# Kernel optimization log

Measured on AMD Instinct MI355X. Metric: run time of the kernel, lower is better.

Reference implementation:

```python
import jax, jax.numpy as jnp
import numpy as np
from jax import lax

KS, STRIDE, DIL, PAD = 3, 1, 1, 1
B, C_IN, C_OUT, D = 1, 16, 16, 64
K = KS ** 3


def setup_inputs():
    key = jax.random.key(0)
    k1, k2, k3 = jax.random.split(key, 3)
    x = jax.random.normal(k1, (B, C_IN, D, D, D), jnp.float32)
    std = 1.0 / float(np.sqrt(C_IN * K))
    kernel = jax.random.uniform(k2, (K, C_IN, C_OUT), jnp.float32, -std, std)
    # module zero-inits pkernel; use small random values so interp path is exercised
    pkernel = jax.random.normal(k3, (K, C_IN, 3 * K), jnp.float32) * 0.01
    return {"x": x, "kernel": kernel, "pkernel": pkernel}


def _deform_conv3d(x, kernel, pkernel):
    Bn, C, Dd, H, W = x.shape
    Kt = kernel.shape[0]
    # offset-predicting conv: pkernel [K, C_in, 3K] -> conv weight [3K, C_in, kd, kh, kw]
    w_off = jnp.transpose(pkernel.reshape(KS, KS, KS, C, 3 * Kt), (4, 3, 0, 1, 2))
    off = lax.conv_general_dilated(
        x, w_off, (STRIDE,) * 3, [(PAD, PAD)] * 3,
        rhs_dilation=(DIL,) * 3,
        dimension_numbers=("NCDHW", "OIDHW", "NCDHW"))
    Do, Ho, Wo = off.shape[2], off.shape[3], off.shape[4]
    off = off.reshape(Bn, Kt, 3, Do, Ho, Wo)  # 3 offset coords per kernel tap

    # base sampling grid: out_pos*stride - pad + tap*dilation, then add predicted offset
    r = jnp.arange(KS)
    tap = jnp.stack(jnp.meshgrid(r, r, r, indexing="ij"), -1).reshape(Kt, 3) * DIL - PAD
    gz = (jnp.arange(Do) * STRIDE).astype(x.dtype)
    gy = (jnp.arange(Ho) * STRIDE).astype(x.dtype)
    gx = (jnp.arange(Wo) * STRIDE).astype(x.dtype)
    cz = gz[None, None, :, None, None] + tap[None, :, 0, None, None, None] + off[:, :, 0]
    cy = gy[None, None, None, :, None] + tap[None, :, 1, None, None, None] + off[:, :, 1]
    cx = gx[None, None, None, None, :] + tap[None, :, 2, None, None, None] + off[:, :, 2]

    x_flat = x.reshape(Bn, C, Dd * H * W)

    def gather(idx):  # idx [B,K,Do,Ho,Wo] int32 -> [B,C,K,Do,Ho,Wo]
        g = jax.vmap(lambda xf, ix: xf[:, ix.reshape(-1)])(x_flat, idx)
        return g.reshape(Bn, C, Kt, Do, Ho, Wo)

    z0f = jnp.floor(cz); y0f = jnp.floor(cy); x0f = jnp.floor(cx)
    fz, fy, fx = cz - z0f, cy - y0f, cx - x0f
    z0 = z0f.astype(jnp.int32); y0 = y0f.astype(jnp.int32); x0 = x0f.astype(jnp.int32)

    # trilinear interp: accumulate 8 corners (zero outside volume)
    acc = jnp.zeros((Bn, C, Kt, Do, Ho, Wo), x.dtype)
    for dz in (0, 1):
        for dy in (0, 1):
            for dx in (0, 1):
                zi, yi, xi = z0 + dz, y0 + dy, x0 + dx
                valid = ((zi >= 0) & (zi < Dd) & (yi >= 0) & (yi < H)
                         & (xi >= 0) & (xi < W)).astype(x.dtype)
                w = ((fz if dz else 1.0 - fz) * (fy if dy else 1.0 - fy)
                     * (fx if dx else 1.0 - fx)) * valid
                idx = (jnp.clip(zi, 0, Dd - 1) * (H * W)
                       + jnp.clip(yi, 0, H - 1) * W + jnp.clip(xi, 0, W - 1))
                acc = acc + gather(idx) * w[:, None]

    # weighted sum over taps: kernel [K, C_in, C_out]
    return jnp.einsum("bckdhw,kco->bodhw", acc, kernel)


def reference(x, kernel, pkernel):
    return _deform_conv3d(x, kernel, pkernel)
```

## Files before the change

### kernel.cpp

```cpp
#include <hip/hip_runtime.h>

#define D 64
#define DD 4096
#define DDD 262144
#define K 27

typedef _Float16 half8  __attribute__((ext_vector_type(8)));
typedef _Float16 half2v __attribute__((ext_vector_type(2)));
typedef float    f32x4  __attribute__((ext_vector_type(4)));
typedef float    f32x2  __attribute__((ext_vector_type(2)));
typedef float    f32x16 __attribute__((ext_vector_type(16)));

#define HX 12
#define HY 8
#define HZ 6
#define HROW 12
#define HPLN 96
#define HSP  576
#define CPAD 24

#define WSW_CH (14*6*64)
#define KSW_CH (27*64)
#define KSW_OFF 88064

__device__ inline half2v h2of(half8 v, int d) {
    half2v r; r.x = v[2*d]; r.y = v[2*d+1]; return r;
}

__global__ __launch_bounds__(256) void prep_weights(const float* __restrict__ pk,
                                                    const float* __restrict__ kern,
                                                    _Float16* __restrict__ Wsw,
                                                    _Float16* __restrict__ Ksw) {
    int t = blockIdx.x * 256 + threadIdx.x;
    if (t < WSW_CH) {
        int lane = t & 63;
        int sm = t >> 6;
        int s = sm / 6, mt = sm - 6 * s;
        int m = mt * 16 + (lane & 15);
        int q = lane >> 4;
        half8 w;
#pragma unroll
        for (int j = 0; j < 8; ++j) {
            int k = 32 * s + 8 * q + j;
            int kt = k >> 4, c = k & 15;
            float wv = (kt < K && m < 81) ? pk[kt * 1296 + c * 81 + m] : 0.0f;
            w[j] = (_Float16)wv;
        }
        *(half8*)(Wsw + t * 8) = w;
    } else if (t < WSW_CH + KSW_CH) {
        int u = t - WSW_CH;
        int kt = u >> 6, lane = u & 63;
        int m = lane & 31, kh = lane >> 5;
        half8 w;
#pragma unroll
        for (int j = 0; j < 8; ++j) {
            int c = kh * 8 + j;
            float wv = (m < 16) ? kern[kt * 256 + c * 16 + m] : 0.0f;
            w[j] = (_Float16)wv;
        }
        *(half8*)(Ksw + u * 8) = w;
    }
}

__global__ __launch_bounds__(256, 4) void deform_main(
    const float* __restrict__ x,
    const _Float16* __restrict__ Wsw,
    const _Float16* __restrict__ Ksw,
    float* __restrict__ out)
{
    __shared__ _Float16 s_h[HSP * CPAD];
    __shared__ _Float16 s_off[81 * 64];

    const int tid  = threadIdx.x;
    const int lane = tid & 63;
    const int wave = __builtin_amdgcn_readfirstlane(tid >> 6);

    const int bx0 = blockIdx.x * 8;
    const int by0 = blockIdx.y * 4;
    const int bz0 = blockIdx.z * 2;

    for (int i = tid; i < HSP; i += 256) {
        int z = i / HPLN;
        int r = i - z * HPLN;
        int y = r / HROW;
        int xx = r - y * HROW;
        int gz = bz0 - 2 + z, gy = by0 - 2 + y, gx = bx0 - 2 + xx;
        bool in = (unsigned)gz < D && (unsigned)gy < D && (unsigned)gx < D;
        half8 a = {}, b = {};
        if (in) {
            const float* p = x + (gz * DD + gy * D + gx);
#pragma unroll
            for (int c = 0; c < 8; ++c) a[c] = (_Float16)p[c * DDD];
#pragma unroll
            for (int c = 0; c < 8; ++c) b[c] = (_Float16)p[(c + 8) * DDD];
        }
        *(half8*)(s_h + i * CPAD)     = a;
        *(half8*)(s_h + i * CPAD + 8) = b;
    }
    __syncthreads();

    {
        const int n = lane & 15, q = lane >> 4;
        const int vtz = wave >> 1;
        const int vty = 2 * (wave & 1) + (n >> 3);
        const int vtx = n & 7;
        f32x4 acc[6] = {};
        for (int s = 0; s < 14; ++s) {
            int kt = 2 * s + (q >> 1);
            int ktc = (kt < K) ? kt : 0;
            int kd = ktc / 9, kh = (ktc / 3) % 3, kw = ktc % 3;
            int idx = (vtz + kd + 1) * HPLN + (vty + kh + 1) * HROW + (vtx + kw + 1);
            half8 bfrag = *(const half8*)(s_h + idx * CPAD + (q & 1) * 8);
#pragma unroll
            for (int mt = 0; mt < 6; ++mt) {
                half8 afrag = *(const half8*)(Wsw + ((s * 6 + mt) * 64 + lane) * 8);
                acc[mt] = __builtin_amdgcn_mfma_f32_16x16x32_f16(afrag, bfrag, acc[mt], 0, 0, 0);
            }
        }
        const int v = wave * 16 + n;
#pragma unroll
        for (int mt = 0; mt < 6; ++mt)
#pragma unroll
            for (int r = 0; r < 4; ++r) {
                int o = mt * 16 + q * 4 + r;
                if (o < 81) s_off[o * 64 + v] = (_Float16)acc[mt][r];
            }
    }
    __syncthreads();

    const int l31 = lane & 31, lh = lane >> 5;
    const int h = wave & 1;
    const int kpar = wave >> 1;
    const int v = h * 32 + l31;
    const int tx = v & 7, ty = (v >> 3) & 3, tz = h;
    const int gz = bz0 + tz, gy = by0 + ty, gx = bx0 + tx;

    f32x16 acc2 = {};

    for (int k2 = 0; k2 < 14; ++k2) {
        const int kt = 2 * k2 + kpar;
        if (kt >= K) break;
        const int kd = kt / 9, kh = (kt / 3) % 3, kw = kt % 3;
        float cz = (float)(gz + kd - 1) + (float)s_off[(3 * kt + 0) * 64 + v];
        float cy = (float)(gy + kh - 1) + (float)s_off[(3 * kt + 1) * 64 + v];
        float cx = (float)(gx + kw - 1) + (float)s_off[(3 * kt + 2) * 64 + v];
        float zf = floorf(cz), yf = floorf(cy), xf = floorf(cx);
        float fz = cz - zf, fy = cy - yf, fx = cx - xf;
        int z0 = (int)zf, y0 = (int)yf, x0 = (int)xf;
        int hz0 = z0 - bz0 + 2, hy0 = y0 - by0 + 2, hx0 = x0 - bx0 + 2;

        half2v val2[4] = {};
        if ((unsigned)hz0 < (unsigned)(HZ - 1) && (unsigned)hy0 < (unsigned)(HY - 1)
            && (unsigned)hx0 < (unsigned)(HX - 1)) {
#pragma unroll
            for (int dz = 0; dz < 2; ++dz) {
                float wz = dz ? fz : 1.0f - fz;
#pragma unroll
                for (int dy = 0; dy < 2; ++dy) {
                    float wzy = wz * (dy ? fy : 1.0f - fy);
#pragma unroll
                    for (int dx = 0; dx < 2; ++dx) {
                        float w = wzy * (dx ? fx : 1.0f - fx);
                        int idx = (hz0 + dz) * HPLN + (hy0 + dy) * HROW + (hx0 + dx);
                        half8 cc = *(const half8*)(s_h + idx * CPAD + lh * 8);
                        _Float16 wh = (_Float16)w;
                        half2v w2; w2.x = wh; w2.y = wh;
#pragma unroll
                        for (int d = 0; d < 4; ++d)
                            val2[d] += w2 * h2of(cc, d);
                    }
                }
            }
        } else {
            f32x2 valf[4] = {};
#pragma unroll
            for (int dz = 0; dz < 2; ++dz) {
                int zi = z0 + dz;
                float wz = dz ? fz : 1.0f - fz;
#pragma unroll
                for (int dy = 0; dy < 2; ++dy) {
                    int yi = y0 + dy;
                    float wzy = wz * (dy ? fy : 1.0f - fy);
#pragma unroll
                    for (int dx = 0; dx < 2; ++dx) {
                        int xi = x0 + dx;
                        if ((unsigned)zi < D && (unsigned)yi < D && (unsigned)xi < D) {
                            float w = wzy * (dx ? fx : 1.0f - fx);
                            int base = zi * DD + yi * D + xi;
#pragma unroll
                            for (int d = 0; d < 4; ++d) {
                                valf[d].x += w * x[(lh * 8 + 2 * d)     * DDD + base];
                                valf[d].y += w * x[(lh * 8 + 2 * d + 1) * DDD + base];
                            }
                        }
                    }
                }
            }
#pragma unroll
            for (int d = 0; d < 4; ++d) {
                val2[d].x = (_Float16)valf[d].x;
                val2[d].y = (_Float16)valf[d].y;
            }
        }

        half8 bf;
#pragma unroll
        for (int d = 0; d < 4; ++d) { bf[2*d] = val2[d].x; bf[2*d+1] = val2[d].y; }
        half8 af = *(const half8*)(Ksw + (kt * 64 + lane) * 8);
        acc2 = __builtin_amdgcn_mfma_f32_32x32x16_f16(af, bf, acc2, 0, 0, 0);
    }

    __syncthreads();
    float* s_red = (float*)s_h;
#pragma unroll
    for (int r = 0; r < 8; ++r) {
        int o = (r & 3) + 8 * (r >> 2) + 4 * lh;
        s_red[(wave * 32 + l31) * 17 + o] = acc2[r];
    }
    __syncthreads();

#pragma unroll
    for (int j = 0; j < 4; ++j) {
        int o = wave * 4 + j;
        float s = s_red[lane * 17 + o] + s_red[(64 + lane) * 17 + o];
        out[o * DDD + (bz0 + (lane >> 5)) * DD + (by0 + ((lane >> 3) & 3)) * D
            + (bx0 + (lane & 7))] = s;
    }
}

extern "C" void kernel_launch(void* const* d_in, const int* in_sizes, int n_in,
                              void* d_out, int out_size, void* d_ws, size_t ws_size,
                              hipStream_t stream) {
    const float* x    = (const float*)d_in[0];
    const float* kern = (const float*)d_in[1];
    const float* pk   = (const float*)d_in[2];
    float* out = (float*)d_out;

    _Float16* Wsw = (_Float16*)d_ws;
    _Float16* Ksw = (_Float16*)((char*)d_ws + KSW_OFF);

    prep_weights<<<28, 256, 0, stream>>>(pk, kern, Wsw, Ksw);
    deform_main<<<dim3(8, 16, 32), 256, 0, stream>>>(x, Wsw, Ksw, out);
}
```

Baseline: 163.8 us.

## Use 16x16x32 MFMA for output stage, removing LDS reduction and padding

Measured after the change: 155.5 us. -5.1%, faster.

```diff
diff --git a/kernel.cpp b/kernel.cpp
--- a/kernel.cpp
+++ b/kernel.cpp
@@ -9,7 +9,6 @@
 typedef _Float16 half2v __attribute__((ext_vector_type(2)));
 typedef float    f32x4  __attribute__((ext_vector_type(4)));
 typedef float    f32x2  __attribute__((ext_vector_type(2)));
-typedef float    f32x16 __attribute__((ext_vector_type(16)));
 
 #define HX 12
 #define HY 8
@@ -17,11 +16,12 @@
 #define HROW 12
 #define HPLN 96
 #define HSP  576
-#define CPAD 24
+#define CPAD 16
+#define OSTR 72
 
 #define WSW_CH (14*6*64)
-#define KSW_CH (27*64)
-#define KSW_OFF 88064
+#define KSW_CH (14*64)
+#define KSW_OFF 86016
 
 __device__ inline half2v h2of(half8 v, int d) {
     half2v r; r.x = v[2*d]; r.y = v[2*d+1]; return r;
@@ -49,27 +49,28 @@
         *(half8*)(Wsw + t * 8) = w;
     } else if (t < WSW_CH + KSW_CH) {
         int u = t - WSW_CH;
-        int kt = u >> 6, lane = u & 63;
-        int m = lane & 31, kh = lane >> 5;
+        int s = u >> 6, lane = u & 63;
+        int o = lane & 15, q = lane >> 4;
         half8 w;
 #pragma unroll
         for (int j = 0; j < 8; ++j) {
-            int c = kh * 8 + j;
-            float wv = (m < 16) ? kern[kt * 256 + c * 16 + m] : 0.0f;
+            int k = q * 8 + j;
+            int kt = 2 * s + (k >> 4), c = k & 15;
+            float wv = (kt < K) ? kern[kt * 256 + c * 16 + o] : 0.0f;
             w[j] = (_Float16)wv;
         }
         *(half8*)(Ksw + u * 8) = w;
     }
 }
 
-__global__ __launch_bounds__(256, 4) void deform_main(
+__global__ __launch_bounds__(256, 5) void deform_main(
     const float* __restrict__ x,
     const _Float16* __restrict__ Wsw,
     const _Float16* __restrict__ Ksw,
     float* __restrict__ out)
 {
     __shared__ _Float16 s_h[HSP * CPAD];
-    __shared__ _Float16 s_off[81 * 64];
+    __shared__ _Float16 s_off[81 * OSTR];
 
     const int tid  = threadIdx.x;
     const int lane = tid & 63;
@@ -99,17 +100,19 @@
     }
     __syncthreads();
 
+    const int n = lane & 15, q = lane >> 4;
+    const int tz = wave >> 1;
+    const int ty = 2 * (wave & 1) + (n >> 3);
+    const int tx = n & 7;
+    const int v = wave * 16 + n;
+
     {
-        const int n = lane & 15, q = lane >> 4;
-        const int vtz = wave >> 1;
-        const int vty = 2 * (wave & 1) + (n >> 3);
-        const int vtx = n & 7;
         f32x4 acc[6] = {};
         for (int s = 0; s < 14; ++s) {
             int kt = 2 * s + (q >> 1);
             int ktc = (kt < K) ? kt : 0;
             int kd = ktc / 9, kh = (ktc / 3) % 3, kw = ktc % 3;
-            int idx = (vtz + kd + 1) * HPLN + (vty + kh + 1) * HROW + (vtx + kw + 1);
+            int idx = (tz + kd + 1) * HPLN + (ty + kh + 1) * HROW + (tx + kw + 1);
             half8 bfrag = *(const half8*)(s_h + idx * CPAD + (q & 1) * 8);
 #pragma unroll
             for (int mt = 0; mt < 6; ++mt) {
@@ -117,33 +120,28 @@
                 acc[mt] = __builtin_amdgcn_mfma_f32_16x16x32_f16(afrag, bfrag, acc[mt], 0, 0, 0);
             }
         }
-        const int v = wave * 16 + n;
 #pragma unroll
         for (int mt = 0; mt < 6; ++mt)
 #pragma unroll
             for (int r = 0; r < 4; ++r) {
                 int o = mt * 16 + q * 4 + r;
-                if (o < 81) s_off[o * 64 + v] = (_Float16)acc[mt][r];
+                if (o < 81) s_off[o * OSTR + v] = (_Float16)acc[mt][r];
             }
     }
     __syncthreads();
 
-    const int l31 = lane & 31, lh = lane >> 5;
-    const int h = wave & 1;
-    const int kpar = wave >> 1;
-    const int v = h * 32 + l31;
-    const int tx = v & 7, ty = (v >> 3) & 3, tz = h;
     const int gz = bz0 + tz, gy = by0 + ty, gx = bx0 + tx;
-
-    f32x16 acc2 = {};
-
-    for (int k2 = 0; k2 < 14; ++k2) {
-        const int kt = 2 * k2 + kpar;
-        if (kt >= K) break;
+    const int cbase = (q & 1) * 8;
+
+    f32x4 acc2 = {};
+
+    for (int s = 0; s < 14; ++s) {
+        const int ktr = 2 * s + (q >> 1);
+        const int kt = (ktr < K) ? ktr : K - 1;
         const int kd = kt / 9, kh = (kt / 3) % 3, kw = kt % 3;
-        float cz = (float)(gz + kd - 1) + (float)s_off[(3 * kt + 0) * 64 + v];
-        float cy = (float)(gy + kh - 1) + (float)s_off[(3 * kt + 1) * 64 + v];
-        float cx = (float)(gx + kw - 1) + (float)s_off[(3 * kt + 2) * 64 + v];
+        float cz = (float)(gz + kd - 1) + (float)s_off[(3 * kt + 0) * OSTR + v];
+        float cy = (float)(gy + kh - 1) + (float)s_off[(3 * kt + 1) * OSTR + v];
+        float cx = (float)(gx + kw - 1) + (float)s_off[(3 * kt + 2) * OSTR + v];
         float zf = floorf(cz), yf = floorf(cy), xf = floorf(cx);
         float fz = cz - zf, fy = cy - yf, fx = cx - xf;
         int z0 = (int)zf, y0 = (int)yf, x0 = (int)xf;
@@ -162,7 +160,7 @@
                     for (int dx = 0; dx < 2; ++dx) {
                         float w = wzy * (dx ? fx : 1.0f - fx);
                         int idx = (hz0 + dz) * HPLN + (hy0 + dy) * HROW + (hx0 + dx);
-                        half8 cc = *(const half8*)(s_h + idx * CPAD + lh * 8);
+                        half8 cc = *(const half8*)(s_h + idx * CPAD + cbase);
                         _Float16 wh = (_Float16)w;
                         half2v w2; w2.x = wh; w2.y = wh;
 #pragma unroll
@@ -189,8 +187,8 @@
                             int base = zi * DD + yi * D + xi;
 #pragma unroll
                             for (int d = 0; d < 4; ++d) {
-                                valf[d].x += w * x[(lh * 8 + 2 * d)     * DDD + base];
-                                valf[d].y += w * x[(lh * 8 + 2 * d + 1) * DDD + base];
+                                valf[d].x += w * x[(cbase + 2 * d)     * DDD + base];
+                                valf[d].y += w * x[(cbase + 2 * d + 1) * DDD + base];
                             }
                         }
                     }
@@ -206,25 +204,15 @@
         half8 bf;
 #pragma unroll
         for (int d = 0; d < 4; ++d) { bf[2*d] = val2[d].x; bf[2*d+1] = val2[d].y; }
-        half8 af = *(const half8*)(Ksw + (kt * 64 + lane) * 8);
-        acc2 = __builtin_amdgcn_mfma_f32_32x32x16_f16(af, bf, acc2, 0, 0, 0);
-    }
-
-    __syncthreads();
-    float* s_red = (float*)s_h;
-#pragma unroll
-    for (int r = 0; r < 8; ++r) {
-        int o = (r & 3) + 8 * (r >> 2) + 4 * lh;
-        s_red[(wave * 32 + l31) * 17 + o] = acc2[r];
-    }
-    __syncthreads();
-
-#pragma unroll
-    for (int j = 0; j < 4; ++j) {
-        int o = wave * 4 + j;
-        float s = s_red[lane * 17 + o] + s_red[(64 + lane) * 17 + o];
-        out[o * DDD + (bz0 + (lane >> 5)) * DD + (by0 + ((lane >> 3) & 3)) * D
-            + (bx0 + (lane & 7))] = s;
+        half8 af = *(const half8*)(Ksw + (s * 64 + lane) * 8);
+        acc2 = __builtin_amdgcn_mfma_f32_16x16x32_f16(af, bf, acc2, 0, 0, 0);
+    }
+
+    const int opos = gz * DD + gy * D + gx;
+#pragma unroll
+    for (int r = 0; r < 4; ++r) {
+        int o = q * 4 + r;
+        out[o * DDD + opos] = acc2[r];
     }
 }
 
@@ -239,6 +227,6 @@
     _Float16* Wsw = (_Float16*)d_ws;
     _Float16* Ksw = (_Float16*)((char*)d_ws + KSW_OFF);
 
-    prep_weights<<<28, 256, 0, stream>>>(pk, kern, Wsw, Ksw);
+    prep_weights<<<25, 256, 0, stream>>>(pk, kern, Wsw, Ksw);
     deform_main<<<dim3(8, 16, 32), 256, 0, stream>>>(x, Wsw, Ksw, out);
 }
```
